# Kernel optimization log

Measured on AMD Instinct MI355X. Metric: run time of the kernel, lower is better.

The kernel has to match this reference:

```python
import jax, jax.numpy as jnp
import numpy as np

EMB = 1024
HEADS = 16
DH = EMB // HEADS
EPS = 1e-5


def _layernorm(x, w, b):
    mean = jnp.mean(x, axis=-1, keepdims=True)
    var = jnp.mean((x - mean) ** 2, axis=-1, keepdims=True)  # unbiased=False
    return w * (x - mean) / jnp.sqrt(var + EPS) + b


def _gelu_tanh(x):
    c = jnp.sqrt(jnp.asarray(2.0 / jnp.pi, x.dtype))
    return 0.5 * x * (1.0 + jnp.tanh(c * (x + 0.044715 * x ** 3)))


def setup_inputs() -> dict:
    key = jax.random.key(0)
    ks = jax.random.split(key, 8)
    B, N = 2, 2048
    s = lambda fan_in: 1.0 / np.sqrt(fan_in)
    # weights stored as [in, out] (torch Linear applied as x @ W.T == x @ W_here)
    return {
        "x": jax.random.normal(ks[0], (B, N, EMB), jnp.float32),
        "ln1_w": jnp.ones((EMB,), jnp.float32),
        "ln1_b": jnp.zeros((EMB,), jnp.float32),
        "w_qkv": jax.random.normal(ks[1], (EMB, 3 * EMB), jnp.float32) * s(EMB),  # qkv_bias=False
        "w_attn_proj": jax.random.normal(ks[2], (EMB, EMB), jnp.float32) * s(EMB),
        "b_attn_proj": jnp.zeros((EMB,), jnp.float32),
        "ln2_w": jnp.ones((EMB,), jnp.float32),
        "ln2_b": jnp.zeros((EMB,), jnp.float32),
        "w_fc": jax.random.normal(ks[3], (EMB, 4 * EMB), jnp.float32) * s(EMB),
        "b_fc": jnp.zeros((4 * EMB,), jnp.float32),
        "w_proj": jax.random.normal(ks[4], (4 * EMB, EMB), jnp.float32) * s(4 * EMB),
        "b_proj": jnp.zeros((EMB,), jnp.float32),
    }


def reference(x, ln1_w, ln1_b, w_qkv, w_attn_proj, b_attn_proj,
              ln2_w, ln2_b, w_fc, b_fc, w_proj, b_proj):
    B, N, _ = x.shape
    # --- attention sublayer (pre-LN) ---
    h = _layernorm(x, ln1_w, ln1_b)
    qkv = h @ w_qkv  # [B,N,3E]
    q, k, v = jnp.split(qkv, 3, axis=-1)
    # [B,H,N,Dh]
    q = q.reshape(B, N, HEADS, DH).transpose(0, 2, 1, 3)
    k = k.reshape(B, N, HEADS, DH).transpose(0, 2, 1, 3)
    v = v.reshape(B, N, HEADS, DH).transpose(0, 2, 1, 3)
    scores = jnp.einsum("bhqd,bhkd->bhqk", q, k) * (DH ** -0.5)
    causal = jnp.tril(jnp.ones((N, N), bool))
    scores = jnp.where(causal, scores, -jnp.inf)
    attn = jax.nn.softmax(scores, axis=-1)  # attn_pdrop=0 (eval)
    ctx = jnp.einsum("bhqk,bhkd->bhqd", attn, v)
    ctx = ctx.transpose(0, 2, 1, 3).reshape(B, N, EMB)
    x = x + (ctx @ w_attn_proj + b_attn_proj)  # resid_pdrop=0
    # --- MLP sublayer (pre-LN) ---
    h = _layernorm(x, ln2_w, ln2_b)
    h = _gelu_tanh(h @ w_fc + b_fc)
    x = x + (h @ w_proj + b_proj)
    return x
```

## Files before the change

kernel.cpp:

```cpp
#include <hip/hip_runtime.h>
#include <stdint.h>

#define EMB 1024
#define NHEAD 16
#define DH 64
#define SEQ 2048
#define NTOK 4096

typedef __attribute__((ext_vector_type(8))) short s16x8;
typedef __attribute__((ext_vector_type(4))) short s16x4;
typedef __attribute__((ext_vector_type(4))) float f32x4;
typedef __attribute__((ext_vector_type(4))) unsigned short u16x4;

__device__ __forceinline__ unsigned short f2bf(float f){
    union { float f; unsigned int u; } v; v.f = f;
    unsigned int r = v.u + 0x7fffu + ((v.u >> 16) & 1u);
    return (unsigned short)(r >> 16);
}

__device__ __forceinline__ f32x4 mfma16(s16x8 a, s16x8 b, f32x4 c){
    return __builtin_amdgcn_mfma_f32_16x16x32_bf16(a, b, c, 0, 0, 0);
}

__device__ __forceinline__ void gload16(const void* g, void* l){
    __builtin_amdgcn_global_load_lds((const __attribute__((address_space(1))) void*)g,
                                     (__attribute__((address_space(3))) void*)l, 16, 0, 0);
}

__device__ __forceinline__ s16x8 cat8(s16x4 a, s16x4 b){
    s16x8 r;
    r[0]=a[0]; r[1]=a[1]; r[2]=a[2]; r[3]=a[3];
    r[4]=b[0]; r[5]=b[1]; r[6]=b[2]; r[7]=b[3];
    return r;
}

__device__ __forceinline__ unsigned cvtpk(float lo, float hi){
    unsigned r;
    asm("v_cvt_pk_bf16_f32 %0, %1, %2" : "=v"(r) : "v"(lo), "v"(hi));
    return r;
}

__device__ __forceinline__ s16x8 qscale(s16x8 q){
    s16x8 r;
    #pragma unroll
    for (int e = 0; e < 8; ++e){
        union { float f; unsigned u; } v;
        v.u = ((unsigned)(unsigned short)q[e]) << 16;
        v.f *= 0.125f;
        r[e] = (short)f2bf(v.f);
    }
    return r;
}

__global__ __launch_bounds__(256) void convT_kernel(const float* __restrict__ in,
                                                    unsigned short* __restrict__ out,
                                                    int R, int C){
    __shared__ float tile[32][33];
    const int c0 = blockIdx.x * 32, r0 = blockIdx.y * 32;
    const int tx = threadIdx.x, ty = threadIdx.y;
    #pragma unroll
    for (int k = 0; k < 4; ++k)
        tile[ty*4+k][tx] = in[(long)(r0 + ty*4 + k) * C + c0 + tx];
    __syncthreads();
    #pragma unroll
    for (int k = 0; k < 4; ++k)
        out[(long)(c0 + ty*4 + k) * R + r0 + tx] = f2bf(tile[tx][ty*4+k]);
}

__global__ __launch_bounds__(256) void vT_kernel(const unsigned short* __restrict__ qkv,
                                                 unsigned short* __restrict__ vtg){
    __shared__ unsigned short tile[64*64];
    const int bh = blockIdx.y, b = bh >> 4, h = bh & 15;
    const int n0 = blockIdx.x * 64;
    const int t = threadIdx.x;
    const int nr = t >> 3, c0 = (t & 7) * 8;
    #pragma unroll
    for (int hh = 0; hh < 2; ++hh){
        const int n = nr + hh*32;
        uint4 vv = *(const uint4*)&qkv[(long)(b*SEQ + n0 + n)*3072 + 2048 + h*64 + c0];
        *(uint4*)((char*)tile + n*128 + ((c0*2) ^ (((n>>3)&7)<<4))) = vv;
    }
    __syncthreads();
    #pragma unroll
    for (int hh = 0; hh < 2; ++hh){
        const int d = nr + hh*32;
        union { unsigned short u[8]; uint4 v; } tmp;
        #pragma unroll
        for (int j = 0; j < 8; ++j){
            const int n = c0 + j;
            tmp.u[j] = *(const unsigned short*)((char*)tile + n*128 + ((d*2) ^ (((n>>3)&7)<<4)));
        }
        *(uint4*)&vtg[((long)bh*64 + d)*2048 + n0 + c0] = tmp.v;
    }
}

__global__ __launch_bounds__(256) void ln_kernel(const float* __restrict__ x,
                                                 const float* __restrict__ w,
                                                 const float* __restrict__ b,
                                                 unsigned short* __restrict__ out){
    const int row = blockIdx.x, tid = threadIdx.x;
    const float4 v = ((const float4*)(x + (long)row * EMB))[tid];
    float s  = v.x + v.y + v.z + v.w;
    float ss = v.x*v.x + v.y*v.y + v.z*v.z + v.w*v.w;
    #pragma unroll
    for (int off = 32; off >= 1; off >>= 1){
        s  += __shfl_xor(s,  off, 64);
        ss += __shfl_xor(ss, off, 64);
    }
    __shared__ float ps[4], pss[4];
    const int wv = tid >> 6;
    if ((tid & 63) == 0){ ps[wv] = s; pss[wv] = ss; }
    __syncthreads();
    s  = ps[0] + ps[1] + ps[2] + ps[3];
    ss = pss[0] + pss[1] + pss[2] + pss[3];
    const float mean = s * (1.0f/EMB);
    const float var  = ss * (1.0f/EMB) - mean*mean;
    const float rstd = rsqrtf(var + 1e-5f);
    const float4 wv4 = ((const float4*)w)[tid];
    const float4 bv4 = ((const float4*)b)[tid];
    u16x4 o;
    o[0] = f2bf((v.x - mean) * rstd * wv4.x + bv4.x);
    o[1] = f2bf((v.y - mean) * rstd * wv4.y + bv4.y);
    o[2] = f2bf((v.z - mean) * rstd * wv4.z + bv4.z);
    o[3] = f2bf((v.w - mean) * rstd * wv4.w + bv4.w);
    *(u16x4*)(out + (long)row * EMB + tid * 4) = o;
}

__global__ __launch_bounds__(256) void red_kernel(const float* __restrict__ p0,
                                                  const float* __restrict__ p1,
                                                  const float* __restrict__ bias,
                                                  const float* __restrict__ resid,
                                                  float* __restrict__ out, int N){
    const long i = ((long)blockIdx.x * 256 + threadIdx.x) * 4;
    const float4 a = *(const float4*)(p0 + i);
    const float4 b = *(const float4*)(p1 + i);
    const float4 r = *(const float4*)(resid + i);
    const float4 bb = *(const float4*)(bias + ((int)i & (N - 1)));
    float4 o;
    o.x = a.x + b.x + r.x + bb.x;
    o.y = a.y + b.y + r.y + bb.y;
    o.z = a.z + b.z + r.z + bb.z;
    o.w = a.w + b.w + r.w + bb.w;
    *(float4*)(out + i) = o;
}

template<int EPI, int SK>
__global__ __launch_bounds__(256, 2) void gemm4_kernel(const unsigned short* __restrict__ A,
                                                       const unsigned short* __restrict__ Bt,
                                                       const float* __restrict__ bias,
                                                       void* __restrict__ out0,
                                                       void* __restrict__ out1,
                                                       int M, int N, int K){
    __shared__ unsigned short As[2][128*64];
    __shared__ unsigned short Bs[2][128*64];
    const int tid = threadIdx.x, lane = tid & 63, w = tid >> 6;
    const int lm = lane & 15, g = lane >> 4;
    const int wr = w >> 1, wc = w & 1;

    const int gx = gridDim.x;
    const int nwg = gx * gridDim.y;
    int id = blockIdx.y * gx + blockIdx.x;
    id = (id & 7) * (nwg >> 3) + (id >> 3);
    const int m0 = (id / gx) * 128, n0 = (id % gx) * 128;
    const int kz = (SK > 1) ? blockIdx.z : 0;
    const int kbase = kz * (K / SK);
    const int nkt = (K / SK) / 64;

    const int r8 = tid >> 3;
    const int src = (((tid & 7) * 16) ^ ((r8 & 7) << 4)) >> 1;
    char* AsB = (char*)&As[0][0];
    char* BsB = (char*)&Bs[0][0];

    auto stage = [&](int bu, int kt){
        #pragma unroll
        for (int p = 0; p < 4; ++p)
            gload16(&A[(long)(m0 + p*32 + r8) * K + kt + src], AsB + bu*16384 + p*4096 + tid*16);
        #pragma unroll
        for (int p = 0; p < 4; ++p)
            gload16(&Bt[(long)(n0 + p*32 + r8) * K + kt + src], BsB + bu*16384 + p*4096 + tid*16);
    };

    f32x4 zero = {0.0f, 0.0f, 0.0f, 0.0f};
    f32x4 acc[4][4];
    #pragma unroll
    for (int i = 0; i < 4; ++i)
        #pragma unroll
        for (int j = 0; j < 4; ++j) acc[i][j] = zero;

    stage(0, kbase);
    int cur = 0;
    const int axor = (lm & 7) << 4;
    for (int t = 0; t < nkt; ++t){
        if (t + 1 < nkt){
            stage(cur ^ 1, kbase + (t + 1) * 64);
            asm volatile("s_waitcnt vmcnt(8)" ::: "memory");
        } else {
            asm volatile("s_waitcnt vmcnt(0)" ::: "memory");
        }
        __builtin_amdgcn_s_barrier();
        asm volatile("" ::: "memory");
        const char* Ab = AsB + cur*16384;
        const char* Bb = BsB + cur*16384;
        #pragma unroll
        for (int kk = 0; kk < 2; ++kk){
            s16x8 af[4], bf[4];
            #pragma unroll
            for (int i = 0; i < 4; ++i)
                af[i] = *(const s16x8*)(Ab + (wr*64 + i*16 + lm)*128 + ((kk*64 + g*16) ^ axor));
            #pragma unroll
            for (int j = 0; j < 4; ++j)
                bf[j] = *(const s16x8*)(Bb + (wc*64 + j*16 + lm)*128 + ((kk*64 + g*16) ^ axor));
            asm volatile("s_waitcnt lgkmcnt(0)" ::: "memory");
            __builtin_amdgcn_sched_barrier(0);
            __builtin_amdgcn_s_setprio(1);
            #pragma unroll
            for (int i = 0; i < 4; ++i)
                #pragma unroll
                for (int j = 0; j < 4; ++j)
                    acc[i][j] = mfma16(af[i], bf[j], acc[i][j]);
            __builtin_amdgcn_s_setprio(0);
        }
        asm volatile("" ::: "memory");
        __builtin_amdgcn_s_barrier();
        asm volatile("" ::: "memory");
        cur ^= 1;
    }

    float* po = (SK > 1 && kz == 1) ? (float*)out1 : (float*)out0;
    #pragma unroll
    for (int i = 0; i < 4; ++i){
        #pragma unroll
        for (int r = 0; r < 4; ++r){
            const int row = m0 + wr*64 + i*16 + 4*g + r;
            #pragma unroll
            for (int j = 0; j < 4; ++j){
                const int col = n0 + wc*64 + j*16 + lm;
                const float v = acc[i][j][r];
                if (EPI == 0){
                    ((unsigned short*)out0)[(long)row * N + col] = f2bf(v);
                } else if (EPI == 2){
                    const float xx = v + bias[col];
                    const float z = 0.7978845608f * (xx + 0.044715f * xx * xx * xx);
                    const float gg = xx / (1.0f + __expf(-2.0f * z));
                    ((unsigned short*)out0)[(long)row * N + col] = f2bf(gg);
                } else {
                    po[(long)row * N + col] = v;
                }
            }
        }
    }
}

template<int EPI, int BM, int BN, int WR, int WC, int SK>
__global__ __launch_bounds__(WR*WC*64) void gemm_kernel(const unsigned short* __restrict__ A,
                                                        const unsigned short* __restrict__ Bt,
                                                        const float* __restrict__ bias,
                                                        const float* __restrict__ resid,
                                                        void* __restrict__ out0,
                                                        void* __restrict__ out1,
                                                        int M, int N, int K){
    constexpr int NW = WR * WC;
    constexpr int NT = NW * 64;
    constexpr int FI = BM / (WR * 16);
    constexpr int FJ = BN / (WC * 16);
    __shared__ unsigned short As[2][BM * 32];
    __shared__ unsigned short Bs[2][BN * 32];
    const int tid  = threadIdx.x;
    const int lane = tid & 63, w = tid >> 6;
    const int lm = lane & 15, g = lane >> 4;
    const int wr = w / WC, wc = w % WC;

    const int gx = gridDim.x;
    const int nwg = gx * gridDim.y;
    int id = blockIdx.y * gx + blockIdx.x;
    id = (id & 7) * (nwg >> 3) + (id >> 3);
    const int m0 = (id / gx) * BM, n0 = (id % gx) * BN;
    const int kz = (SK > 1) ? blockIdx.z : 0;
    const int kbase = kz * (K / SK);

    f32x4 zero = {0.0f, 0.0f, 0.0f, 0.0f};
    f32x4 acc[FI][FJ];
    #pragma unroll
    for (int i = 0; i < FI; ++i)
        #pragma unroll
        for (int j = 0; j < FJ; ++j) acc[i][j] = zero;

    auto stage = [&](int kt, int bu){
        #pragma unroll
        for (int p = 0; p < BM/(NT/4); ++p)
            gload16(&A[(long)(m0 + p*(NT/4) + (tid>>2)) * K + kt + (tid&3)*8],
                    (char*)&As[bu][0] + p*(NT*16) + tid*16);
        #pragma unroll
        for (int p = 0; p < BN/(NT/4); ++p)
            gload16(&Bt[(long)(n0 + p*(NT/4) + (tid>>2)) * K + kt + (tid&3)*8],
                    (char*)&Bs[bu][0] + p*(NT*16) + tid*16);
    };

    stage(kbase, 0);
    int cur = 0;
    const int nkt = (K / SK) / 32;
    for (int t = 0; t < nkt; ++t){
        __syncthreads();
        if (t + 1 < nkt) stage(kbase + (t+1)*32, cur ^ 1);
        s16x8 af[FI], bf[FJ];
        #pragma unroll
        for (int i = 0; i < FI; ++i)
            af[i] = *(const s16x8*)&As[cur][(wr*(FI*16) + i*16 + lm)*32 + g*8];
        #pragma unroll
        for (int j = 0; j < FJ; ++j)
            bf[j] = *(const s16x8*)&Bs[cur][(wc*(FJ*16) + j*16 + lm)*32 + g*8];
        #pragma unroll
        for (int i = 0; i < FI; ++i)
            #pragma unroll
            for (int j = 0; j < FJ; ++j)
                acc[i][j] = mfma16(af[i], bf[j], acc[i][j]);
        cur ^= 1;
    }

    float* po = (SK > 1 && kz == 1) ? (float*)out1 : (float*)out0;
    #pragma unroll
    for (int i = 0; i < FI; ++i){
        #pragma unroll
        for (int r = 0; r < 4; ++r){
            const int row = m0 + wr*(FI*16) + i*16 + 4*g + r;
            #pragma unroll
            for (int j = 0; j < FJ; ++j){
                const int col = n0 + wc*(FJ*16) + j*16 + lm;
                const float v = acc[i][j][r];
                if (EPI == 0){
                    ((unsigned short*)out0)[(long)row * N + col] = f2bf(v);
                } else if (EPI == 1){
                    ((float*)out0)[(long)row * N + col] =
                        v + bias[col] + resid[(long)row * N + col];
                } else if (EPI == 2){
                    const float xx = v + bias[col];
                    const float z = 0.7978845608f * (xx + 0.044715f * xx * xx * xx);
                    const float gg = xx / (1.0f + __expf(-2.0f * z));
                    ((unsigned short*)out0)[(long)row * N + col] = f2bf(gg);
                } else {
                    po[(long)row * N + col] = v;
                }
            }
        }
    }
}

__global__ __launch_bounds__(256) void attn_kernel(const unsigned short* __restrict__ qkv,
                                                   const unsigned short* __restrict__ vtg,
                                                   unsigned short* __restrict__ ctx){
    __shared__ unsigned short Ks[3][4096];
    __shared__ unsigned short Vs[3][4096];
    int id0 = blockIdx.y * 16 + blockIdx.x;
    const int id = (id0 & 7) * 64 + (id0 >> 3);
    const int pair = id & 15, bh = id >> 4;
    const int b = bh >> 4, h = bh & 15;
    const int tid = threadIdx.x, lane = tid & 63, w = tid >> 6;
    const int lm = lane & 15, g = lane >> 4;
    const long qkvb = (long)b * SEQ * 3072;
    const unsigned short* kglob = qkv + qkvb + 1024 + h*64;
    const unsigned short* vglob = vtg + (long)bh * 64 * 2048;

    const int srow = tid >> 3;
    const int soff = (tid & 7) * 16;
    const int swz = (lm & 7) << 4;
    f32x4 zero = {0.0f, 0.0f, 0.0f, 0.0f};

    #pragma unroll 1
    for (int grp = 0; grp < 2; ++grp){
        const int qg = (grp == 0) ? pair : (31 - pair);
        const int q0 = qg * 64;
        const int nt = qg + 1;
        const int qrow = q0 + w*16 + lm;

        const unsigned short* qrp = qkv + qkvb + (long)qrow*3072 + h*64;
        const s16x8 qf0 = qscale(*(const s16x8*)(qrp + g*8));
        const s16x8 qf1 = qscale(*(const s16x8*)(qrp + 32 + g*8));

        f32x4 o[4];
        #pragma unroll
        for (int d = 0; d < 4; ++d) o[d] = zero;
        float lsum = 0.0f;

        auto stageKV = [&](int t, int bu){
            const int kv0 = t * 64;
            #pragma unroll
            for (int hh = 0; hh < 2; ++hh){
                const int row = srow + hh*32;
                const int sw  = soff ^ ((row & 7) << 4);
                gload16(kglob + (long)(kv0 + row)*3072 + (sw >> 1),
                        (char*)&Ks[bu][0] + hh*4096 + w*1024);
                gload16(vglob + (long)row*2048 + kv0 + (sw >> 1),
                        (char*)&Vs[bu][0] + hh*4096 + w*1024);
            }
        };
        auto qkt = [&](int bu, f32x4* sc){
            const char* Kb = (const char*)&Ks[bu][0];
            #pragma unroll
            for (int s = 0; s < 4; ++s){
                const char* rp = Kb + (s*16 + lm)*128;
                s16x8 kf0 = *(const s16x8*)(rp + ((g*16) ^ swz));
                s16x8 kf1 = *(const s16x8*)(rp + ((64 + g*16) ^ swz));
                f32x4 a = mfma16(kf0, qf0, zero);
                sc[s] = mfma16(kf1, qf1, a);
            }
        };

        __builtin_amdgcn_s_barrier();
        asm volatile("" ::: "memory");
        stageKV(0, 0);
        if (nt > 1){
            stageKV(1, 1);
            asm volatile("s_waitcnt vmcnt(4)" ::: "memory");
        } else {
            asm volatile("s_waitcnt vmcnt(0)" ::: "memory");
        }
        __builtin_amdgcn_s_barrier();
        asm volatile("" ::: "memory");

        f32x4 sc[4], scN[4];
        qkt(0, sc);

        #pragma unroll 1
        for (int t = 0; t < nt; ++t){
            const bool more = (t + 1 < nt);
            if (more){
                asm volatile("s_waitcnt vmcnt(0)" ::: "memory");
                __builtin_amdgcn_s_barrier();
                asm volatile("" ::: "memory");
                if (t + 2 < nt) stageKV(t + 2, (t + 2) % 3);
                qkt((t + 1) % 3, scN);
            }

            if (t == nt - 1){
                #pragma unroll
                for (int s = 0; s < 4; ++s)
                    #pragma unroll
                    for (int r = 0; r < 4; ++r)
                        if (s*16 + 4*g + r > w*16 + lm) sc[s][r] = -1e30f;
            }
            float pp[4][4];
            #pragma unroll
            for (int s = 0; s < 4; ++s)
                #pragma unroll
                for (int r = 0; r < 4; ++r){
                    const float e = __expf(sc[s][r]);
                    pp[s][r] = e;
                    lsum += e;
                }

            union { unsigned u[4]; s16x8 v; } P0, P1;
            P0.u[0] = cvtpk(pp[0][0], pp[0][1]);
            P0.u[1] = cvtpk(pp[0][2], pp[0][3]);
            P0.u[2] = cvtpk(pp[1][0], pp[1][1]);
            P0.u[3] = cvtpk(pp[1][2], pp[1][3]);
            P1.u[0] = cvtpk(pp[2][0], pp[2][1]);
            P1.u[1] = cvtpk(pp[2][2], pp[2][3]);
            P1.u[2] = cvtpk(pp[3][0], pp[3][1]);
            P1.u[3] = cvtpk(pp[3][2], pp[3][3]);

            const char* Vb = (const char*)&Vs[t % 3][0];
            #pragma unroll
            for (int d = 0; d < 4; ++d){
                const char* vrp = Vb + (d*16 + lm)*128;
                s16x4 a0 = *(const s16x4*)(vrp + ((g*8) ^ swz));
                s16x4 a1 = *(const s16x4*)(vrp + ((32 + g*8) ^ swz));
                o[d] = mfma16(cat8(a0, a1), P0.v, o[d]);
                s16x4 b0 = *(const s16x4*)(vrp + ((64 + g*8) ^ swz));
                s16x4 b1 = *(const s16x4*)(vrp + ((96 + g*8) ^ swz));
                o[d] = mfma16(cat8(b0, b1), P1.v, o[d]);
            }
            if (more){
                #pragma unroll
                for (int s4 = 0; s4 < 4; ++s4) sc[s4] = scN[s4];
            }
        }

        lsum += __shfl_xor(lsum, 16, 64);
        lsum += __shfl_xor(lsum, 32, 64);
        const float inv = 1.0f / lsum;
        unsigned short* cw = ctx + (long)(b*SEQ + qrow)*EMB + h*DH + 4*g;
        #pragma unroll
        for (int d = 0; d < 4; ++d){
            u16x4 ov;
            ov[0] = f2bf(o[d][0]*inv); ov[1] = f2bf(o[d][1]*inv);
            ov[2] = f2bf(o[d][2]*inv); ov[3] = f2bf(o[d][3]*inv);
            *(u16x4*)(cw + d*16) = ov;
        }
    }
}

extern "C" void kernel_launch(void* const* d_in, const int* in_sizes, int n_in,
                              void* d_out, int out_size, void* d_ws, size_t ws_size,
                              hipStream_t stream){
    const float* x     = (const float*)d_in[0];
    const float* ln1_w = (const float*)d_in[1];
    const float* ln1_b = (const float*)d_in[2];
    const float* w_qkv = (const float*)d_in[3];
    const float* w_ap  = (const float*)d_in[4];
    const float* b_ap  = (const float*)d_in[5];
    const float* ln2_w = (const float*)d_in[6];
    const float* ln2_b = (const float*)d_in[7];
    const float* w_fc  = (const float*)d_in[8];
    const float* b_fc  = (const float*)d_in[9];
    const float* w_pr  = (const float*)d_in[10];
    const float* b_pr  = (const float*)d_in[11];
    float* out = (float*)d_out;

    char* ws = (char*)d_ws;
    unsigned short* wqkvT = (unsigned short*)(ws + 0);
    unsigned short* wapT  = (unsigned short*)(ws + 6291456);
    unsigned short* wfcT  = (unsigned short*)(ws + 8388608);
    unsigned short* wprT  = (unsigned short*)(ws + 16777216);
    unsigned short* h1    = (unsigned short*)(ws + 25165824);
    unsigned short* vtg   = (unsigned short*)(ws + 25165824);
    unsigned short* qkv   = (unsigned short*)(ws + 33554432);
    unsigned short* ctx   = (unsigned short*)(ws + 58720256);
    float*          x1    = (float*)(ws + 67108864);
    unsigned short* h2    = (unsigned short*)(ws + 83886080);
    unsigned short* afc   = (unsigned short*)(ws + 92274688);
    float* pp0 = (float*)(ws + 0);
    float* pp1 = (float*)(ws + 25165824);

    dim3 b32(32, 8, 1);
    convT_kernel<<<dim3(3072/32, 1024/32), b32, 0, stream>>>(w_qkv, wqkvT, 1024, 3072);
    convT_kernel<<<dim3(1024/32, 1024/32), b32, 0, stream>>>(w_ap,  wapT,  1024, 1024);
    convT_kernel<<<dim3(4096/32, 1024/32), b32, 0, stream>>>(w_fc,  wfcT,  1024, 4096);
    convT_kernel<<<dim3(1024/32, 4096/32), b32, 0, stream>>>(w_pr,  wprT,  4096, 1024);

    ln_kernel<<<NTOK, 256, 0, stream>>>(x, ln1_w, ln1_b, h1);

    gemm4_kernel<0,1><<<dim3(3072/128, NTOK/128), 256, 0, stream>>>(
        h1, wqkvT, nullptr, qkv, nullptr, NTOK, 3072, 1024);

    vT_kernel<<<dim3(SEQ/64, 32), 256, 0, stream>>>(qkv, vtg);

    attn_kernel<<<dim3(16, 32), 256, 0, stream>>>(qkv, vtg, ctx);

    gemm_kernel<1,128,64,2,2,1><<<dim3(1024/64, NTOK/128), 256, 0, stream>>>(
        ctx, wapT, b_ap, x, x1, nullptr, NTOK, 1024, 1024);

    ln_kernel<<<NTOK, 256, 0, stream>>>(x1, ln2_w, ln2_b, h2);

    gemm4_kernel<2,1><<<dim3(4096/128, NTOK/128), 256, 0, stream>>>(
        h2, wfcT, b_fc, afc, nullptr, NTOK, 4096, 1024);

    gemm4_kernel<3,2><<<dim3(1024/128, NTOK/128, 2), 256, 0, stream>>>(
        afc, wprT, nullptr, pp0, pp1, NTOK, 1024, 4096);
    red_kernel<<<NTOK*EMB/1024, 256, 0, stream>>>(pp0, pp1, b_pr, x1, out, EMB);
}
```

Measured before the change: 236.5 us.

## Add XCD-aware 2D tile grouping and vectorized transposed-MFMA epilogue in gemm4

Replaces the simple XCD round-robin remap with a parameterized mapping that gives each of the 8 XCDs a contiguous rectangular patch of output tiles (xr by yr). The goal is more L2 reuse of A and B tiles within an XCD. It also swaps the MFMA operand order so each lane holds four consecutive columns of one row, which lets the epilogue write 4-wide vector stores (u16x4 or float4) instead of scalar stores. The mapping depends on the grid dimensions dividing evenly by the chosen xr/yr values.

```diff
diff --git a/kernel.cpp b/kernel.cpp
--- a/kernel.cpp
+++ b/kernel.cpp
@@ -150,7 +150,8 @@
                                                        const float* __restrict__ bias,
                                                        void* __restrict__ out0,
                                                        void* __restrict__ out1,
-                                                       int M, int N, int K){
+                                                       int M, int N, int K,
+                                                       int xr, int yr){
     __shared__ unsigned short As[2][128*64];
     __shared__ unsigned short Bs[2][128*64];
     const int tid = threadIdx.x, lane = tid & 63, w = tid >> 6;
@@ -158,10 +159,11 @@
     const int wr = w >> 1, wc = w & 1;
 
     const int gx = gridDim.x;
-    const int nwg = gx * gridDim.y;
-    int id = blockIdx.y * gx + blockIdx.x;
-    id = (id & 7) * (nwg >> 3) + (id >> 3);
-    const int m0 = (id / gx) * 128, n0 = (id % gx) * 128;
+    const int o = blockIdx.y * gx + blockIdx.x;
+    const int x = o & 7, j = o >> 3;
+    const int nrx = gx / xr;
+    const int m0 = ((x / nrx) * yr + j / xr) * 128;
+    const int n0 = ((x % nrx) * xr + j % xr) * 128;
     const int kz = (SK > 1) ? blockIdx.z : 0;
     const int kbase = kz * (K / SK);
     const int nkt = (K / SK) / 64;
@@ -185,7 +187,7 @@
     #pragma unroll
     for (int i = 0; i < 4; ++i)
         #pragma unroll
-        for (int j = 0; j < 4; ++j) acc[i][j] = zero;
+        for (int jj = 0; jj < 4; ++jj) acc[i][jj] = zero;
 
     stage(0, kbase);
     int cur = 0;
@@ -208,16 +210,16 @@
             for (int i = 0; i < 4; ++i)
                 af[i] = *(const s16x8*)(Ab + (wr*64 + i*16 + lm)*128 + ((kk*64 + g*16) ^ axor));
             #pragma unroll
-            for (int j = 0; j < 4; ++j)
-                bf[j] = *(const s16x8*)(Bb + (wc*64 + j*16 + lm)*128 + ((kk*64 + g*16) ^ axor));
+            for (int jj = 0; jj < 4; ++jj)
+                bf[jj] = *(const s16x8*)(Bb + (wc*64 + jj*16 + lm)*128 + ((kk*64 + g*16) ^ axor));
             asm volatile("s_waitcnt lgkmcnt(0)" ::: "memory");
             __builtin_amdgcn_sched_barrier(0);
             __builtin_amdgcn_s_setprio(1);
             #pragma unroll
             for (int i = 0; i < 4; ++i)
                 #pragma unroll
-                for (int j = 0; j < 4; ++j)
-                    acc[i][j] = mfma16(af[i], bf[j], acc[i][j]);
+                for (int jj = 0; jj < 4; ++jj)
+                    acc[i][jj] = mfma16(bf[jj], af[i], acc[i][jj]);
             __builtin_amdgcn_s_setprio(0);
         }
         asm volatile("" ::: "memory");
@@ -229,23 +231,27 @@
     float* po = (SK > 1 && kz == 1) ? (float*)out1 : (float*)out0;
     #pragma unroll
     for (int i = 0; i < 4; ++i){
-        #pragma unroll
-        for (int r = 0; r < 4; ++r){
-            const int row = m0 + wr*64 + i*16 + 4*g + r;
-            #pragma unroll
-            for (int j = 0; j < 4; ++j){
-                const int col = n0 + wc*64 + j*16 + lm;
-                const float v = acc[i][j][r];
-                if (EPI == 0){
-                    ((unsigned short*)out0)[(long)row * N + col] = f2bf(v);
-                } else if (EPI == 2){
-                    const float xx = v + bias[col];
+        const int row = m0 + wr*64 + i*16 + lm;
+        #pragma unroll
+        for (int jj = 0; jj < 4; ++jj){
+            const int col = n0 + wc*64 + jj*16 + 4*g;
+            const f32x4 v = acc[i][jj];
+            if (EPI == 0){
+                u16x4 ov;
+                ov[0] = f2bf(v[0]); ov[1] = f2bf(v[1]);
+                ov[2] = f2bf(v[2]); ov[3] = f2bf(v[3]);
+                *(u16x4*)&((unsigned short*)out0)[(long)row * N + col] = ov;
+            } else if (EPI == 2){
+                u16x4 ov;
+                #pragma unroll
+                for (int r = 0; r < 4; ++r){
+                    const float xx = v[r] + bias[col + r];
                     const float z = 0.7978845608f * (xx + 0.044715f * xx * xx * xx);
-                    const float gg = xx / (1.0f + __expf(-2.0f * z));
-                    ((unsigned short*)out0)[(long)row * N + col] = f2bf(gg);
-                } else {
-                    po[(long)row * N + col] = v;
+                    ov[r] = f2bf(xx / (1.0f + __expf(-2.0f * z)));
                 }
+                *(u16x4*)&((unsigned short*)out0)[(long)row * N + col] = ov;
+            } else {
+                *(float4*)&po[(long)row * N + col] = *(const float4*)&v;
             }
         }
     }
@@ -530,7 +536,7 @@
     ln_kernel<<<NTOK, 256, 0, stream>>>(x, ln1_w, ln1_b, h1);
 
     gemm4_kernel<0,1><<<dim3(3072/128, NTOK/128), 256, 0, stream>>>(
-        h1, wqkvT, nullptr, qkv, nullptr, NTOK, 3072, 1024);
+        h1, wqkvT, nullptr, qkv, nullptr, NTOK, 3072, 1024, 12, 8);
 
     vT_kernel<<<dim3(SEQ/64, 32), 256, 0, stream>>>(qkv, vtg);
 
@@ -542,9 +548,9 @@
     ln_kernel<<<NTOK, 256, 0, stream>>>(x1, ln2_w, ln2_b, h2);
 
     gemm4_kernel<2,1><<<dim3(4096/128, NTOK/128), 256, 0, stream>>>(
-        h2, wfcT, b_fc, afc, nullptr, NTOK, 4096, 1024);
+        h2, wfcT, b_fc, afc, nullptr, NTOK, 4096, 1024, 16, 8);
 
     gemm4_kernel<3,2><<<dim3(1024/128, NTOK/128, 2), 256, 0, stream>>>(
-        afc, wprT, nullptr, pp0, pp1, NTOK, 1024, 4096);
+        afc, wprT, nullptr, pp0, pp1, NTOK, 1024, 4096, 8, 4);
     red_kernel<<<NTOK*EMB/1024, 256, 0, stream>>>(pp0, pp1, b_pr, x1, out, EMB);
 }
```

New measurement: 241.2 us. Within noise of the previous version (+2.0%).

## Merge weight transposes into one launch and add 128x64 swizzled GEMM for MLP proj

Applied to the files above, without the earlier changes.

Combines the four weight convert-transpose launches into a single kernel that picks its matrix from the block index, removing launch overhead and tail gaps. Adds a new gemm5 kernel with 128x64 tiles, BK=64, XOR-swizzled LDS, double-buffered async loads, launch bounds allowing 3 blocks per CU, and grouped block ordering for L2 reuse. The new kernel replaces gemm4 for the split-K down projection. Smaller tiles give more blocks and better occupancy but less reuse per block.

```diff
diff --git a/kernel.cpp b/kernel.cpp
--- a/kernel.cpp
+++ b/kernel.cpp
@@ -52,11 +52,18 @@
     return r;
 }
 
-__global__ __launch_bounds__(256) void convT_kernel(const float* __restrict__ in,
-                                                    unsigned short* __restrict__ out,
-                                                    int R, int C){
+__global__ __launch_bounds__(256) void convT4_kernel(const float* __restrict__ q, unsigned short* __restrict__ qo,
+                                                     const float* __restrict__ a, unsigned short* __restrict__ ao,
+                                                     const float* __restrict__ f, unsigned short* __restrict__ fo,
+                                                     const float* __restrict__ p, unsigned short* __restrict__ po){
     __shared__ float tile[32][33];
-    const int c0 = blockIdx.x * 32, r0 = blockIdx.y * 32;
+    int id = blockIdx.x;
+    const float* in; unsigned short* out; int R, C, bx, by;
+    if (id < 3072)      { in = q; out = qo; R = 1024; C = 3072; bx = id % 96;  by = id / 96;  }
+    else if (id < 4096) { id -= 3072; in = a; out = ao; R = 1024; C = 1024; bx = id % 32; by = id / 32; }
+    else if (id < 8192) { id -= 4096; in = f; out = fo; R = 1024; C = 4096; bx = id % 128; by = id / 128; }
+    else                { id -= 8192; in = p; out = po; R = 4096; C = 1024; bx = id % 32; by = id / 32; }
+    const int c0 = bx * 32, r0 = by * 32;
     const int tx = threadIdx.x, ty = threadIdx.y;
     #pragma unroll
     for (int k = 0; k < 4; ++k)
@@ -246,6 +253,115 @@
                 } else {
                     po[(long)row * N + col] = v;
                 }
+            }
+        }
+    }
+}
+
+template<int EPI, int SK>
+__global__ __launch_bounds__(256, 3) void gemm5_kernel(const unsigned short* __restrict__ A,
+                                                       const unsigned short* __restrict__ Bt,
+                                                       const float* __restrict__ bias,
+                                                       const float* __restrict__ resid,
+                                                       float* __restrict__ out0,
+                                                       float* __restrict__ out1,
+                                                       int M, int N, int K,
+                                                       int xr, int yr){
+    __shared__ unsigned short As[2][128*64];
+    __shared__ unsigned short Bs[2][64*64];
+    const int tid = threadIdx.x, lane = tid & 63, w = tid >> 6;
+    const int lm = lane & 15, g = lane >> 4;
+    const int wr = w >> 1, wc = w & 1;
+
+    const int gx = gridDim.x;
+    const int o = blockIdx.y * gx + blockIdx.x;
+    const int x = o & 7, j = o >> 3;
+    const int nrx = gx / xr;
+    const int m0 = ((x / nrx) * yr + j / xr) * 128;
+    const int n0 = ((x % nrx) * xr + j % xr) * 64;
+    const int kz = (SK > 1) ? blockIdx.z : 0;
+    const int kbase = kz * (K / SK);
+    const int nkt = (K / SK) / 64;
+
+    const int r8 = tid >> 3;
+    const int src = (((tid & 7) * 16) ^ ((r8 & 7) << 4)) >> 1;
+    char* AsB = (char*)&As[0][0];
+    char* BsB = (char*)&Bs[0][0];
+
+    auto stage = [&](int bu, int kt){
+        #pragma unroll
+        for (int p = 0; p < 4; ++p)
+            gload16(&A[(long)(m0 + p*32 + r8) * K + kt + src], AsB + bu*16384 + p*4096 + tid*16);
+        #pragma unroll
+        for (int p = 0; p < 2; ++p)
+            gload16(&Bt[(long)(n0 + p*32 + r8) * K + kt + src], BsB + bu*8192 + p*4096 + tid*16);
+    };
+
+    f32x4 zero = {0.0f, 0.0f, 0.0f, 0.0f};
+    f32x4 acc[4][2];
+    #pragma unroll
+    for (int i = 0; i < 4; ++i)
+        #pragma unroll
+        for (int jj = 0; jj < 2; ++jj) acc[i][jj] = zero;
+
+    stage(0, kbase);
+    int cur = 0;
+    const int axor = (lm & 7) << 4;
+    for (int t = 0; t < nkt; ++t){
+        if (t + 1 < nkt){
+            stage(cur ^ 1, kbase + (t + 1) * 64);
+            asm volatile("s_waitcnt vmcnt(6)" ::: "memory");
+        } else {
+            asm volatile("s_waitcnt vmcnt(0)" ::: "memory");
+        }
+        __builtin_amdgcn_s_barrier();
+        asm volatile("" ::: "memory");
+        const char* Ab = AsB + cur*16384;
+        const char* Bb = BsB + cur*8192;
+        #pragma unroll
+        for (int kk = 0; kk < 2; ++kk){
+            s16x8 af[4], bf[2];
+            #pragma unroll
+            for (int i = 0; i < 4; ++i)
+                af[i] = *(const s16x8*)(Ab + (wr*64 + i*16 + lm)*128 + ((kk*64 + g*16) ^ axor));
+            #pragma unroll
+            for (int jj = 0; jj < 2; ++jj)
+                bf[jj] = *(const s16x8*)(Bb + (wc*32 + jj*16 + lm)*128 + ((kk*64 + g*16) ^ axor));
+            asm volatile("s_waitcnt lgkmcnt(0)" ::: "memory");
+            __builtin_amdgcn_sched_barrier(0);
+            __builtin_amdgcn_s_setprio(1);
+            #pragma unroll
+            for (int i = 0; i < 4; ++i)
+                #pragma unroll
+                for (int jj = 0; jj < 2; ++jj)
+                    acc[i][jj] = mfma16(bf[jj], af[i], acc[i][jj]);
+            __builtin_amdgcn_s_setprio(0);
+        }
+        asm volatile("" ::: "memory");
+        __builtin_amdgcn_s_barrier();
+        asm volatile("" ::: "memory");
+        cur ^= 1;
+    }
+
+    float* po = (SK > 1 && kz == 1) ? out1 : out0;
+    #pragma unroll
+    for (int i = 0; i < 4; ++i){
+        const int row = m0 + wr*64 + i*16 + lm;
+        #pragma unroll
+        for (int jj = 0; jj < 2; ++jj){
+            const int col = n0 + wc*32 + jj*16 + 4*g;
+            const f32x4 v = acc[i][jj];
+            if (EPI == 1){
+                const float4 bb = *(const float4*)&bias[col];
+                const float4 rr = *(const float4*)&resid[(long)row * N + col];
+                float4 ov;
+                ov.x = v[0] + bb.x + rr.x;
+                ov.y = v[1] + bb.y + rr.y;
+                ov.z = v[2] + bb.z + rr.z;
+                ov.w = v[3] + bb.w + rr.w;
+                *(float4*)&out0[(long)row * N + col] = ov;
+            } else {
+                *(float4*)&po[(long)row * N + col] = *(const float4*)&v;
             }
         }
     }
@@ -521,11 +637,8 @@
     float* pp0 = (float*)(ws + 0);
     float* pp1 = (float*)(ws + 25165824);
 
-    dim3 b32(32, 8, 1);
-    convT_kernel<<<dim3(3072/32, 1024/32), b32, 0, stream>>>(w_qkv, wqkvT, 1024, 3072);
-    convT_kernel<<<dim3(1024/32, 1024/32), b32, 0, stream>>>(w_ap,  wapT,  1024, 1024);
-    convT_kernel<<<dim3(4096/32, 1024/32), b32, 0, stream>>>(w_fc,  wfcT,  1024, 4096);
-    convT_kernel<<<dim3(1024/32, 4096/32), b32, 0, stream>>>(w_pr,  wprT,  4096, 1024);
+    convT4_kernel<<<12288, dim3(32, 8, 1), 0, stream>>>(
+        w_qkv, wqkvT, w_ap, wapT, w_fc, wfcT, w_pr, wprT);
 
     ln_kernel<<<NTOK, 256, 0, stream>>>(x, ln1_w, ln1_b, h1);
 
@@ -544,7 +657,7 @@
     gemm4_kernel<2,1><<<dim3(4096/128, NTOK/128), 256, 0, stream>>>(
         h2, wfcT, b_fc, afc, nullptr, NTOK, 4096, 1024);
 
-    gemm4_kernel<3,2><<<dim3(1024/128, NTOK/128, 2), 256, 0, stream>>>(
-        afc, wprT, nullptr, pp0, pp1, NTOK, 1024, 4096);
+    gemm5_kernel<3,2><<<dim3(1024/64, NTOK/128, 2), 256, 0, stream>>>(
+        afc, wprT, nullptr, nullptr, pp0, pp1, NTOK, 1024, 4096, 8, 8);
     red_kernel<<<NTOK*EMB/1024, 256, 0, stream>>>(pp0, pp1, b_pr, x1, out, EMB);
 }
```

Measured after the change: 248.8 us. +5.2%, slower.
